# Kernel tuning notes

Measured on AMD Instinct MI355X. Metric: run time of the kernel, lower is better.

The kernel has to match this reference:

```python
import jax, jax.numpy as jnp
import numpy as np

LAMBDA_PROTO = 0.5
EPS = 1e-12  # F.normalize eps


def setup_inputs() -> dict:
    key = jax.random.key(0)
    k1, k2, k3 = jax.random.split(key, 3)
    N, D, C = 262144, 128, 64
    emb = jax.random.normal(k1, (N, D), dtype=jnp.float32)
    logits = jax.random.normal(k2, (N, C), dtype=jnp.float32)
    labels = jax.random.randint(k3, (N,), 0, C, dtype=jnp.int64)
    return {"emb": emb, "logits": logits, "labels": labels}


def reference(emb, logits, labels):
    N, D = emb.shape
    C = logits.shape[1]

    # F.normalize(emb, dim=1): x / max(||x||, eps)
    nrm = jnp.sqrt(jnp.sum(emb * emb, axis=1, keepdims=True))
    z = emb / jnp.maximum(nrm, EPS)

    # Cross-entropy (mean reduction, no class weights)
    logp = jax.nn.log_softmax(logits, axis=-1)
    ce = -jnp.mean(jnp.take_along_axis(logp, labels[:, None], axis=1))

    # Per-class stats via segment reduce (single fused pass, no python loop)
    lab = labels.astype(jnp.int32)
    counts = jax.ops.segment_sum(jnp.ones((N,), jnp.float32), lab, num_segments=C)  # [C]
    sums = jax.ops.segment_sum(z, lab, num_segments=C)                               # [C, D]
    sq = jax.ops.segment_sum(jnp.sum(z * z, axis=1), lab, num_segments=C)            # [C]

    safe_n = jnp.maximum(counts, 1.0)
    mu = sums / safe_n[:, None]
    # sum_i ||z_i - mu||^2 = sum_i ||z_i||^2 - n * ||mu||^2
    ssd = sq - counts * jnp.sum(mu * mu, axis=1)
    per_class = ssd / safe_n  # mean over samples of squared distance

    valid = counts > 1.0  # classes with <=1 sample are skipped
    n_valid = jnp.sum(valid.astype(jnp.float32))
    proto_loss = jnp.sum(jnp.where(valid, per_class, 0.0)) / jnp.maximum(n_valid, 1.0)

    return (1.0 - LAMBDA_PROTO) * ce + LAMBDA_PROTO * proto_loss
```

## Files before the change

kernel.cpp:

```cpp
#include <hip/hip_runtime.h>
#include <math.h>

#define N_ROWS 262144
#define D 128
#define C 64
#define NB1 2048
#define RPB1 128
#define SCB 512
#define CSTRIDE 4608
#define PB 1024
#define PT 512
#define TMAX 9
#define OCTW 132

#define OFF_HIST   0
#define OFF_BASES  (NB1 * C)
#define OFF_IDX    (2 * NB1 * C)
#define OFF_CNT    (2 * NB1 * C + C * CSTRIDE)
#define OFF_CEB    (OFF_CNT + C)
#define OFF_OCT    (OFF_CEB + NB1)
#define OFF_RES    (OFF_OCT + PB * OCTW)

__global__ __launch_bounds__(256, 8) void ce_hist_kernel(
    const float* __restrict__ logits, const int* __restrict__ labels,
    float* __restrict__ ceB, int* __restrict__ hist) {
  __shared__ float sCe[4];
  __shared__ int sH[C];
  const int tid = threadIdx.x;
  if (tid < C) sH[tid] = 0;
  __syncthreads();

  const int wave = tid >> 6, lane = tid & 63;
  const int g = lane >> 4, lp = lane & 15;
  const int rowBase = blockIdx.x * RPB1 + wave * 32 + g;
  float ce_acc = 0.f;

  float4 tA, tB;
  int labA = 0, labB = 0;
  tA = *(const float4*)(logits + (size_t)rowBase * C + lp * 4);
  labA = labels[rowBase];
  tB = tA;

#pragma unroll
  for (int it = 0; it < 8; ++it) {
    const float4 t4 = (it & 1) ? tB : tA;
    const int lab = (it & 1) ? labB : labA;
    if (it + 1 < 8) {
      const int row = rowBase + (it + 1) * 4;
      if (it & 1) {
        tA = *(const float4*)(logits + (size_t)row * C + lp * 4);
        labA = labels[row];
      } else {
        tB = *(const float4*)(logits + (size_t)row * C + lp * 4);
        labB = labels[row];
      }
    }
    float p = __expf(t4.x) + __expf(t4.y) + __expf(t4.z) + __expf(t4.w);
    float tl = 0.f;
    if ((lab >> 2) == lp) {
      const int k = lab & 3;
      tl = k == 0 ? t4.x : k == 1 ? t4.y : k == 2 ? t4.z : t4.w;
    }
    p += __shfl_xor(p, 1);  tl += __shfl_xor(tl, 1);
    p += __shfl_xor(p, 2);  tl += __shfl_xor(tl, 2);
    p += __shfl_xor(p, 4);  tl += __shfl_xor(tl, 4);
    p += __shfl_xor(p, 8);  tl += __shfl_xor(tl, 8);
    if (lp == 0) {
      ce_acc += __logf(p) - tl;
      atomicAdd(&sH[lab], 1);
    }
  }
  ce_acc += __shfl_xor(ce_acc, 16);
  ce_acc += __shfl_xor(ce_acc, 32);
  if (lane == 0) sCe[wave] = ce_acc;
  __syncthreads();
  if (tid == 0) ceB[blockIdx.x] = sCe[0] + sCe[1] + sCe[2] + sCe[3];
  if (tid < C) hist[blockIdx.x * C + tid] = sH[tid];
}

__global__ __launch_bounds__(256) void scan_kernel(
    const int* __restrict__ hist, int* __restrict__ bases,
    int* __restrict__ cnts) {
  __shared__ int sA[256], sB[256];
  const int c = blockIdx.x, t = threadIdx.x;
  int h[8], tot = 0;
#pragma unroll
  for (int j = 0; j < 8; ++j) {
    h[j] = hist[(t * 8 + j) * C + c];
    tot += h[j];
  }
  sA[t] = tot;
  __syncthreads();
#pragma unroll
  for (int st = 0; st < 8; ++st) {
    const int off = 1 << st;
    if (st & 1) sA[t] = sB[t] + ((t >= off) ? sB[t - off] : 0);
    else        sB[t] = sA[t] + ((t >= off) ? sA[t - off] : 0);
    __syncthreads();
  }
  const int incl = sA[t];
  int run = incl - tot;
#pragma unroll
  for (int j = 0; j < 8; ++j) {
    bases[(t * 8 + j) * C + c] = run;
    run += h[j];
  }
  if (t == 255) cnts[c] = incl;
}

__global__ __launch_bounds__(512) void scatter_kernel(
    const int* __restrict__ labels, const int* __restrict__ bases,
    int* __restrict__ idx) {
  __shared__ int sCur[C];
  const int t = threadIdx.x, b = blockIdx.x;
  if (t < C) sCur[t] = bases[(b * 4) * C + t];
  __syncthreads();
  const int row = b * 512 + t;
  const int lab = labels[row];
  const int pos = atomicAdd(&sCur[lab], 1);
  idx[lab * CSTRIDE + pos] = row;
}

__global__ __launch_bounds__(PT, 4) void proto_kernel(
    const float* __restrict__ emb, const int* __restrict__ idxArr,
    const int* __restrict__ cnts, float* __restrict__ oct) {
  const int tid = threadIdx.x;
  const int wave = tid >> 6, lane = tid & 63;
  const int g = lane >> 4, lp = lane & 15;
  const int c = blockIdx.x >> 4, o = blockIdx.x & 15;
  const int gg = o * 32 + wave * 4 + g;
  const int n = cnts[c];
  const int nm1 = (n > 0) ? n - 1 : 0;
  const int* ip = idxArr + c * CSTRIDE;

  int rI[TMAX];
#pragma unroll
  for (int t = 0; t < TMAX; ++t) {
    const int e = gg + 512 * t;
    rI[t] = ip[e < nm1 ? e : nm1];
  }

  float4 s0a, s0b, s1a, s1b, s2a, s2b, s3a, s3b, s4a, s4b, s5a, s5b;
  {
    const float* p0 = emb + (size_t)rI[0] * D + lp * 8;
    s0a = *(const float4*)p0;  s0b = *(const float4*)(p0 + 4);
    const float* p1 = emb + (size_t)rI[1] * D + lp * 8;
    s1a = *(const float4*)p1;  s1b = *(const float4*)(p1 + 4);
    const float* p2 = emb + (size_t)rI[2] * D + lp * 8;
    s2a = *(const float4*)p2;  s2b = *(const float4*)(p2 + 4);
    const float* p3 = emb + (size_t)rI[3] * D + lp * 8;
    s3a = *(const float4*)p3;  s3b = *(const float4*)(p3 + 4);
    const float* p4 = emb + (size_t)rI[4] * D + lp * 8;
    s4a = *(const float4*)p4;  s4b = *(const float4*)(p4 + 4);
    const float* p5 = emb + (size_t)rI[5] * D + lp * 8;
    s5a = *(const float4*)p5;  s5b = *(const float4*)(p5 + 4);
  }

  float4 accA = {0.f, 0.f, 0.f, 0.f}, accB = {0.f, 0.f, 0.f, 0.f};
  float cnt = 0.f, sq = 0.f;

#pragma unroll
  for (int t = 0; t < TMAX; ++t) {
    const int r6 = t % 6;
    const float4 ea = r6 == 0 ? s0a : r6 == 1 ? s1a : r6 == 2 ? s2a
                    : r6 == 3 ? s3a : r6 == 4 ? s4a : s5a;
    const float4 eb = r6 == 0 ? s0b : r6 == 1 ? s1b : r6 == 2 ? s2b
                    : r6 == 3 ? s3b : r6 == 4 ? s4b : s5b;
    if (t + 6 < TMAX) {
      const float* pn = emb + (size_t)rI[t + 6] * D + lp * 8;
      if (r6 == 0)      { s0a = *(const float4*)pn; s0b = *(const float4*)(pn + 4); }
      else if (r6 == 1) { s1a = *(const float4*)pn; s1b = *(const float4*)(pn + 4); }
      else              { s2a = *(const float4*)pn; s2b = *(const float4*)(pn + 4); }
    }
    float ss = ea.x * ea.x + ea.y * ea.y + ea.z * ea.z + ea.w * ea.w +
               eb.x * eb.x + eb.y * eb.y + eb.z * eb.z + eb.w * eb.w;
    ss += __shfl_xor(ss, 1);
    ss += __shfl_xor(ss, 2);
    ss += __shfl_xor(ss, 4);
    ss += __shfl_xor(ss, 8);
    const float inv = 1.0f / fmaxf(sqrtf(ss), 1e-12f);
    const bool valid = (gg + 512 * t) < n;
    const float sc = valid ? inv : 0.f;
    accA.x += ea.x * sc;  accA.y += ea.y * sc;
    accA.z += ea.z * sc;  accA.w += ea.w * sc;
    accB.x += eb.x * sc;  accB.y += eb.y * sc;
    accB.z += eb.z * sc;  accB.w += eb.w * sc;
    if (lp == 0) {
      cnt += valid ? 1.f : 0.f;
      sq += valid ? ss * inv * inv : 0.f;
    }
  }

#pragma unroll
  for (int off = 16; off <= 32; off <<= 1) {
    accA.x += __shfl_xor(accA.x, off);  accA.y += __shfl_xor(accA.y, off);
    accA.z += __shfl_xor(accA.z, off);  accA.w += __shfl_xor(accA.w, off);
    accB.x += __shfl_xor(accB.x, off);  accB.y += __shfl_xor(accB.y, off);
    accB.z += __shfl_xor(accB.z, off);  accB.w += __shfl_xor(accB.w, off);
    cnt += __shfl_xor(cnt, off);
    sq += __shfl_xor(sq, off);
  }

  __shared__ float sR[8][OCTW];
  if (lane < 16) {
    *(float4*)&sR[wave][lp * 8] = accA;
    *(float4*)&sR[wave][lp * 8 + 4] = accB;
  }
  if (lane == 0) { sR[wave][128] = cnt; sR[wave][129] = sq; }
  __syncthreads();
  if (tid < 130) {
    float s = 0.f;
#pragma unroll
    for (int w = 0; w < 8; ++w) s += sR[w][tid];
    oct[(size_t)blockIdx.x * OCTW + tid] = s;
  }
}

__global__ __launch_bounds__(128) void class_kernel(
    const float* __restrict__ oct, float* __restrict__ res) {
  __shared__ float sM[2];
  const int c = blockIdx.x, t = threadIdx.x;
  float s = 0.f, n = 0.f, sq = 0.f;
#pragma unroll
  for (int o = 0; o < 16; ++o) {
    const float* f = oct + (size_t)(c * 16 + o) * OCTW;
    s += f[t];
    n += f[128];
    sq += f[129];
  }
  const float safe = fmaxf(n, 1.f);
  const float mu = s / safe;
  float msq = mu * mu;
#pragma unroll
  for (int off = 1; off < 64; off <<= 1) msq += __shfl_xor(msq, off);
  if ((t & 63) == 0) sM[t >> 6] = msq;
  __syncthreads();
  if (t == 0) {
    const float ssd = sq - n * (sM[0] + sM[1]);
    const bool valid = n > 1.f;
    res[c] = valid ? ssd / safe : 0.f;
    res[C + c] = valid ? 1.f : 0.f;
  }
}

__global__ __launch_bounds__(256) void final_kernel(
    const float* __restrict__ ceB, const float* __restrict__ res,
    float* __restrict__ out) {
  __shared__ float sv[4][3];
  const int tid = threadIdx.x, wave = tid >> 6, lane = tid & 63;
  float ce = 0.f;
  for (int i = tid; i < NB1; i += 256) ce += ceB[i];
  float pr = 0.f, nv = 0.f;
  if (wave == 0) { pr = res[lane]; nv = res[C + lane]; }
#pragma unroll
  for (int off = 1; off < 64; off <<= 1) {
    ce += __shfl_xor(ce, off);
    pr += __shfl_xor(pr, off);
    nv += __shfl_xor(nv, off);
  }
  if (lane == 0) { sv[wave][0] = ce; sv[wave][1] = pr; sv[wave][2] = nv; }
  __syncthreads();
  if (tid == 0) {
    const float c2 = sv[0][0] + sv[1][0] + sv[2][0] + sv[3][0];
    const float p2 = sv[0][1] + sv[1][1] + sv[2][1] + sv[3][1];
    const float n2 = sv[0][2] + sv[1][2] + sv[2][2] + sv[3][2];
    out[0] = 0.5f * (c2 / (float)N_ROWS) + 0.5f * (p2 / fmaxf(n2, 1.f));
  }
}

extern "C" void kernel_launch(void* const* d_in, const int* in_sizes, int n_in,
                              void* d_out, int out_size, void* d_ws, size_t ws_size,
                              hipStream_t stream) {
  const float* emb = (const float*)d_in[0];
  const float* logits = (const float*)d_in[1];
  const int* labels = (const int*)d_in[2];
  int* wsi = (int*)d_ws;
  float* wsf = (float*)d_ws;
  float* out = (float*)d_out;

  int* hist = wsi + OFF_HIST;
  int* bases = wsi + OFF_BASES;
  int* idx = wsi + OFF_IDX;
  int* cnts = wsi + OFF_CNT;
  float* ceB = wsf + OFF_CEB;
  float* oct = wsf + OFF_OCT;
  float* res = wsf + OFF_RES;

  ce_hist_kernel<<<NB1, 256, 0, stream>>>(logits, labels, ceB, hist);
  scan_kernel<<<C, 256, 0, stream>>>(hist, bases, cnts);
  scatter_kernel<<<SCB, 512, 0, stream>>>(labels, bases, idx);
  proto_kernel<<<PB, PT, 0, stream>>>(emb, idx, cnts, oct);
  class_kernel<<<C, 128, 0, stream>>>(oct, res);
  final_kernel<<<1, 256, 0, stream>>>(ceB, res, out);
}
```

Measured before the change: 54.63 us.

## Fuse class and final kernels, deepen prefetch, hand-schedule proto gather loads

Merges the per-class reduction and the final reduction into one single-block kernel, which removes one launch. The CE kernel's logits prefetch goes from two to four rows in flight. The scatter kernel now handles two labels per thread, with half as many blocks. The proto kernel issues its gather loads through inline asm with explicit vmcnt waits and scheduling barriers, to keep more memory requests outstanding. The trade-offs are a fragile hand-written schedule and a final kernel that runs the per-class work serially in one block.

```diff
diff --git a/kernel.cpp b/kernel.cpp
--- a/kernel.cpp
+++ b/kernel.cpp
@@ -6,7 +6,7 @@
 #define C 64
 #define NB1 2048
 #define RPB1 128
-#define SCB 512
+#define SCB 256
 #define CSTRIDE 4608
 #define PB 1024
 #define PT 512
@@ -19,7 +19,13 @@
 #define OFF_CNT    (2 * NB1 * C + C * CSTRIDE)
 #define OFF_CEB    (OFF_CNT + C)
 #define OFF_OCT    (OFF_CEB + NB1)
-#define OFF_RES    (OFF_OCT + PB * OCTW)
+
+__device__ __forceinline__ void gload8(float4& a, float4& b, const float* p) {
+  asm volatile("global_load_dwordx4 %0, %2, off\n\t"
+               "global_load_dwordx4 %1, %2, off offset:16"
+               : "=&v"(a), "=&v"(b)
+               : "v"(p));
+}
 
 __global__ __launch_bounds__(256, 8) void ce_hist_kernel(
     const float* __restrict__ logits, const int* __restrict__ labels,
@@ -35,25 +41,29 @@
   const int rowBase = blockIdx.x * RPB1 + wave * 32 + g;
   float ce_acc = 0.f;
 
-  float4 tA, tB;
-  int labA = 0, labB = 0;
-  tA = *(const float4*)(logits + (size_t)rowBase * C + lp * 4);
-  labA = labels[rowBase];
-  tB = tA;
+  float4 tA, tB, tC, tD;
+  int lA, lB, lC, lD;
+  {
+    const float* lg = logits + (size_t)rowBase * C + lp * 4;
+    tA = *(const float4*)(lg + 0 * 4 * C);  lA = labels[rowBase + 0];
+    tB = *(const float4*)(lg + 1 * 4 * C);  lB = labels[rowBase + 4];
+    tC = *(const float4*)(lg + 2 * 4 * C);  lC = labels[rowBase + 8];
+    tD = *(const float4*)(lg + 3 * 4 * C);  lD = labels[rowBase + 12];
+  }
 
 #pragma unroll
   for (int it = 0; it < 8; ++it) {
-    const float4 t4 = (it & 1) ? tB : tA;
-    const int lab = (it & 1) ? labB : labA;
-    if (it + 1 < 8) {
-      const int row = rowBase + (it + 1) * 4;
-      if (it & 1) {
-        tA = *(const float4*)(logits + (size_t)row * C + lp * 4);
-        labA = labels[row];
-      } else {
-        tB = *(const float4*)(logits + (size_t)row * C + lp * 4);
-        labB = labels[row];
-      }
+    const int r4 = it & 3;
+    const float4 t4 = r4 == 0 ? tA : r4 == 1 ? tB : r4 == 2 ? tC : tD;
+    const int lab = r4 == 0 ? lA : r4 == 1 ? lB : r4 == 2 ? lC : lD;
+    if (it + 4 < 8) {
+      const int row = rowBase + (it + 4) * 4;
+      const float4 nt = *(const float4*)(logits + (size_t)row * C + lp * 4);
+      const int nl = labels[row];
+      if (r4 == 0)      { tA = nt; lA = nl; }
+      else if (r4 == 1) { tB = nt; lB = nl; }
+      else if (r4 == 2) { tC = nt; lC = nl; }
+      else              { tD = nt; lD = nl; }
     }
     float p = __expf(t4.x) + __expf(t4.y) + __expf(t4.z) + __expf(t4.w);
     float tl = 0.f;
@@ -113,21 +123,25 @@
     int* __restrict__ idx) {
   __shared__ int sCur[C];
   const int t = threadIdx.x, b = blockIdx.x;
-  if (t < C) sCur[t] = bases[(b * 4) * C + t];
-  __syncthreads();
-  const int row = b * 512 + t;
-  const int lab = labels[row];
-  const int pos = atomicAdd(&sCur[lab], 1);
-  idx[lab * CSTRIDE + pos] = row;
+  if (t < C) sCur[t] = bases[(b * 8) * C + t];
+  __syncthreads();
+  const int row = b * 1024 + t * 2;
+  const int2 l = *(const int2*)(labels + row);
+  const int p0 = atomicAdd(&sCur[l.x], 1);
+  idx[l.x * CSTRIDE + p0] = row;
+  const int p1 = atomicAdd(&sCur[l.y], 1);
+  idx[l.y * CSTRIDE + p1] = row + 1;
 }
 
 __global__ __launch_bounds__(PT, 4) void proto_kernel(
     const float* __restrict__ emb, const int* __restrict__ idxArr,
     const int* __restrict__ cnts, float* __restrict__ oct) {
+  __shared__ float sR[8][OCTW];
   const int tid = threadIdx.x;
   const int wave = tid >> 6, lane = tid & 63;
   const int g = lane >> 4, lp = lane & 15;
-  const int c = blockIdx.x >> 4, o = blockIdx.x & 15;
+  const int b = blockIdx.x;
+  const int c = b >> 4, o = b & 15;
   const int gg = o * 32 + wave * 4 + g;
   const int n = cnts[c];
   const int nm1 = (n > 0) ? n - 1 : 0;
@@ -139,39 +153,22 @@
     const int e = gg + 512 * t;
     rI[t] = ip[e < nm1 ? e : nm1];
   }
+#pragma unroll
+  for (int t = 0; t < TMAX; ++t) asm volatile("" :: "v"(rI[t]));
+  __builtin_amdgcn_sched_barrier(0);
 
   float4 s0a, s0b, s1a, s1b, s2a, s2b, s3a, s3b, s4a, s4b, s5a, s5b;
-  {
-    const float* p0 = emb + (size_t)rI[0] * D + lp * 8;
-    s0a = *(const float4*)p0;  s0b = *(const float4*)(p0 + 4);
-    const float* p1 = emb + (size_t)rI[1] * D + lp * 8;
-    s1a = *(const float4*)p1;  s1b = *(const float4*)(p1 + 4);
-    const float* p2 = emb + (size_t)rI[2] * D + lp * 8;
-    s2a = *(const float4*)p2;  s2b = *(const float4*)(p2 + 4);
-    const float* p3 = emb + (size_t)rI[3] * D + lp * 8;
-    s3a = *(const float4*)p3;  s3b = *(const float4*)(p3 + 4);
-    const float* p4 = emb + (size_t)rI[4] * D + lp * 8;
-    s4a = *(const float4*)p4;  s4b = *(const float4*)(p4 + 4);
-    const float* p5 = emb + (size_t)rI[5] * D + lp * 8;
-    s5a = *(const float4*)p5;  s5b = *(const float4*)(p5 + 4);
-  }
+  gload8(s0a, s0b, emb + (size_t)rI[0] * D + lp * 8);
+  gload8(s1a, s1b, emb + (size_t)rI[1] * D + lp * 8);
+  gload8(s2a, s2b, emb + (size_t)rI[2] * D + lp * 8);
+  gload8(s3a, s3b, emb + (size_t)rI[3] * D + lp * 8);
+  gload8(s4a, s4b, emb + (size_t)rI[4] * D + lp * 8);
+  gload8(s5a, s5b, emb + (size_t)rI[5] * D + lp * 8);
 
   float4 accA = {0.f, 0.f, 0.f, 0.f}, accB = {0.f, 0.f, 0.f, 0.f};
   float cnt = 0.f, sq = 0.f;
 
-#pragma unroll
-  for (int t = 0; t < TMAX; ++t) {
-    const int r6 = t % 6;
-    const float4 ea = r6 == 0 ? s0a : r6 == 1 ? s1a : r6 == 2 ? s2a
-                    : r6 == 3 ? s3a : r6 == 4 ? s4a : s5a;
-    const float4 eb = r6 == 0 ? s0b : r6 == 1 ? s1b : r6 == 2 ? s2b
-                    : r6 == 3 ? s3b : r6 == 4 ? s4b : s5b;
-    if (t + 6 < TMAX) {
-      const float* pn = emb + (size_t)rI[t + 6] * D + lp * 8;
-      if (r6 == 0)      { s0a = *(const float4*)pn; s0b = *(const float4*)(pn + 4); }
-      else if (r6 == 1) { s1a = *(const float4*)pn; s1b = *(const float4*)(pn + 4); }
-      else              { s2a = *(const float4*)pn; s2b = *(const float4*)(pn + 4); }
-    }
+  auto consume = [&](const float4 ea, const float4 eb, const int t) {
     float ss = ea.x * ea.x + ea.y * ea.y + ea.z * ea.z + ea.w * ea.w +
                eb.x * eb.x + eb.y * eb.y + eb.z * eb.z + eb.w * eb.w;
     ss += __shfl_xor(ss, 1);
@@ -189,7 +186,23 @@
       cnt += valid ? 1.f : 0.f;
       sq += valid ? ss * inv * inv : 0.f;
     }
-  }
+  };
+
+#define PSTEP(T, NW, SA, SB)                          \
+  asm volatile("s_waitcnt vmcnt(" #NW ")");           \
+  __builtin_amdgcn_sched_barrier(0);                  \
+  consume(SA, SB, T);
+
+  PSTEP(0, 10, s0a, s0b)  gload8(s0a, s0b, emb + (size_t)rI[6] * D + lp * 8);
+  PSTEP(1, 10, s1a, s1b)  gload8(s1a, s1b, emb + (size_t)rI[7] * D + lp * 8);
+  PSTEP(2, 10, s2a, s2b)  gload8(s2a, s2b, emb + (size_t)rI[8] * D + lp * 8);
+  PSTEP(3, 10, s3a, s3b)
+  PSTEP(4, 8,  s4a, s4b)
+  PSTEP(5, 6,  s5a, s5b)
+  PSTEP(6, 4,  s0a, s0b)
+  PSTEP(7, 2,  s1a, s1b)
+  PSTEP(8, 0,  s2a, s2b)
+#undef PSTEP
 
 #pragma unroll
   for (int off = 16; off <= 32; off <<= 1) {
@@ -201,7 +214,6 @@
     sq += __shfl_xor(sq, off);
   }
 
-  __shared__ float sR[8][OCTW];
   if (lane < 16) {
     *(float4*)&sR[wave][lp * 8] = accA;
     *(float4*)&sR[wave][lp * 8 + 4] = accB;
@@ -212,59 +224,53 @@
     float s = 0.f;
 #pragma unroll
     for (int w = 0; w < 8; ++w) s += sR[w][tid];
-    oct[(size_t)blockIdx.x * OCTW + tid] = s;
-  }
-}
-
-__global__ __launch_bounds__(128) void class_kernel(
-    const float* __restrict__ oct, float* __restrict__ res) {
-  __shared__ float sM[2];
-  const int c = blockIdx.x, t = threadIdx.x;
-  float s = 0.f, n = 0.f, sq = 0.f;
-#pragma unroll
-  for (int o = 0; o < 16; ++o) {
-    const float* f = oct + (size_t)(c * 16 + o) * OCTW;
-    s += f[t];
-    n += f[128];
-    sq += f[129];
-  }
-  const float safe = fmaxf(n, 1.f);
-  const float mu = s / safe;
-  float msq = mu * mu;
-#pragma unroll
-  for (int off = 1; off < 64; off <<= 1) msq += __shfl_xor(msq, off);
-  if ((t & 63) == 0) sM[t >> 6] = msq;
-  __syncthreads();
-  if (t == 0) {
-    const float ssd = sq - n * (sM[0] + sM[1]);
-    const bool valid = n > 1.f;
-    res[c] = valid ? ssd / safe : 0.f;
-    res[C + c] = valid ? 1.f : 0.f;
-  }
-}
-
-__global__ __launch_bounds__(256) void final_kernel(
-    const float* __restrict__ ceB, const float* __restrict__ res,
+    oct[(size_t)b * OCTW + tid] = s;
+  }
+}
+
+__global__ __launch_bounds__(1024) void classfinal_kernel(
+    const float* __restrict__ oct, const float* __restrict__ ceB,
     float* __restrict__ out) {
-  __shared__ float sv[4][3];
+  __shared__ float sPer[C], sVal[C], sCe[16];
   const int tid = threadIdx.x, wave = tid >> 6, lane = tid & 63;
-  float ce = 0.f;
-  for (int i = tid; i < NB1; i += 256) ce += ceB[i];
-  float pr = 0.f, nv = 0.f;
-  if (wave == 0) { pr = res[lane]; nv = res[C + lane]; }
-#pragma unroll
-  for (int off = 1; off < 64; off <<= 1) {
-    ce += __shfl_xor(ce, off);
-    pr += __shfl_xor(pr, off);
-    nv += __shfl_xor(nv, off);
-  }
-  if (lane == 0) { sv[wave][0] = ce; sv[wave][1] = pr; sv[wave][2] = nv; }
+
+  float ce = ceB[tid] + ceB[tid + 1024];
+#pragma unroll
+  for (int off = 1; off < 64; off <<= 1) ce += __shfl_xor(ce, off);
+  if (lane == 0) sCe[wave] = ce;
+
+#pragma unroll
+  for (int q = 0; q < 4; ++q) {
+    const int c = wave * 4 + q;
+    float s0 = 0.f, s1 = 0.f, n = 0.f, sq = 0.f;
+#pragma unroll
+    for (int o = 0; o < 16; ++o) {
+      const float* f = oct + (size_t)(c * 16 + o) * OCTW;
+      s0 += f[lane];
+      s1 += f[64 + lane];
+      n += f[128];
+      sq += f[129];
+    }
+    const float safe = fmaxf(n, 1.f);
+    const float mu0 = s0 / safe, mu1 = s1 / safe;
+    float msq = mu0 * mu0 + mu1 * mu1;
+#pragma unroll
+    for (int off = 1; off < 64; off <<= 1) msq += __shfl_xor(msq, off);
+    if (lane == 0) {
+      const float ssd = sq - n * msq;
+      const bool valid = n > 1.f;
+      sPer[c] = valid ? ssd / safe : 0.f;
+      sVal[c] = valid ? 1.f : 0.f;
+    }
+  }
   __syncthreads();
   if (tid == 0) {
-    const float c2 = sv[0][0] + sv[1][0] + sv[2][0] + sv[3][0];
-    const float p2 = sv[0][1] + sv[1][1] + sv[2][1] + sv[3][1];
-    const float n2 = sv[0][2] + sv[1][2] + sv[2][2] + sv[3][2];
-    out[0] = 0.5f * (c2 / (float)N_ROWS) + 0.5f * (p2 / fmaxf(n2, 1.f));
+    float pr = 0.f, nv = 0.f, c2 = 0.f;
+#pragma unroll
+    for (int c = 0; c < C; ++c) { pr += sPer[c]; nv += sVal[c]; }
+#pragma unroll
+    for (int w = 0; w < 16; ++w) c2 += sCe[w];
+    out[0] = 0.5f * (c2 / (float)N_ROWS) + 0.5f * (pr / fmaxf(nv, 1.f));
   }
 }
 
@@ -284,12 +290,10 @@
   int* cnts = wsi + OFF_CNT;
   float* ceB = wsf + OFF_CEB;
   float* oct = wsf + OFF_OCT;
-  float* res = wsf + OFF_RES;
 
   ce_hist_kernel<<<NB1, 256, 0, stream>>>(logits, labels, ceB, hist);
   scan_kernel<<<C, 256, 0, stream>>>(hist, bases, cnts);
   scatter_kernel<<<SCB, 512, 0, stream>>>(labels, bases, idx);
   proto_kernel<<<PB, PT, 0, stream>>>(emb, idx, cnts, oct);
-  class_kernel<<<C, 128, 0, stream>>>(oct, res);
-  final_kernel<<<1, 256, 0, stream>>>(ceB, res, out);
-}
+  classfinal_kernel<<<1, 1024, 0, stream>>>(oct, ceB, out);
+}
```

Result: slower. 64.44 us (+18.0%).
